# Kernel tuning notes

Measured on AMD Instinct MI355X. Metric: run time of the kernel, lower is better.

Reference implementation:

```python
import jax, jax.numpy as jnp
import numpy as np

EPS = 1e-8  # torch F.cosine_similarity default eps
N, D, K, S = 200000, 512, 32, 1000

def setup_inputs() -> dict:
    key = jax.random.key(0)
    k1, k2, k3 = jax.random.split(key, 3)
    z = jax.random.normal(k1, (N, D), dtype=jnp.float32)
    knn_neighbors = jax.random.randint(k2, (N, K), 0, N)
    sample_indices = jax.random.randint(k3, (S,), 0, N)
    return {"z": z, "knn_neighbors": knn_neighbors, "sample_indices": sample_indices}

def reference(z, knn_neighbors, sample_indices):
    # Gather sampled centers and their neighbor embeddings.
    centers = z[sample_indices]                         # [S, D]
    neigh = z[knn_neighbors[sample_indices]]            # [S, K, D]
    # Cosine similarity along D (torch semantics: dot / max(|a||b|, eps)).
    dot = jnp.einsum('sd,skd->sk', centers, neigh)      # [S, K]
    norm_c = jnp.linalg.norm(centers, axis=-1)          # [S]
    norm_n = jnp.linalg.norm(neigh, axis=-1)            # [S, K]
    cos = dot / jnp.maximum(norm_c[:, None] * norm_n, EPS)
    # Per-center loss 1 - mean cos sim, averaged over sampled centers.
    return jnp.mean(1.0 - jnp.mean(cos, axis=1))
```

## Files before the change

### kernel.cpp

```cpp
#include <hip/hip_runtime.h>
#include <hip/hip_bf16.h>


#define DDIM 512
#define KNN 32
#define EPSV 1e-8f

__global__ __launch_bounds__(256) void ncl_pair_kernel(
    const float* __restrict__ z,
    const int* __restrict__ knn,
    const int* __restrict__ samp,
    float* __restrict__ block_sums) {
    const int b    = blockIdx.x;
    const int s    = b >> 3;
    const int g    = b & 7;
    const int lane = threadIdx.x & 63;
    const int wave = threadIdx.x >> 6;
    const int k    = g * 4 + wave;

    const int cidx = samp[s];
    const int nidx = knn[(size_t)cidx * KNN + k];

    const float4* __restrict__ crow = (const float4*)(z + (size_t)cidx * DDIM);
    const float4* __restrict__ nrow = (const float4*)(z + (size_t)nidx * DDIM);
    const float4 c0 = crow[lane];
    const float4 c1 = crow[64 + lane];
    const float4 n0 = nrow[lane];
    const float4 n1 = nrow[64 + lane];

    float cn = c0.x*c0.x; float dp = c0.x*n0.x; float nn = n0.x*n0.x;
    cn = fmaf(c0.y, c0.y, cn); dp = fmaf(c0.y, n0.y, dp); nn = fmaf(n0.y, n0.y, nn);
    cn = fmaf(c0.z, c0.z, cn); dp = fmaf(c0.z, n0.z, dp); nn = fmaf(n0.z, n0.z, nn);
    cn = fmaf(c0.w, c0.w, cn); dp = fmaf(c0.w, n0.w, dp); nn = fmaf(n0.w, n0.w, nn);
    cn = fmaf(c1.x, c1.x, cn); dp = fmaf(c1.x, n1.x, dp); nn = fmaf(n1.x, n1.x, nn);
    cn = fmaf(c1.y, c1.y, cn); dp = fmaf(c1.y, n1.y, dp); nn = fmaf(n1.y, n1.y, nn);
    cn = fmaf(c1.z, c1.z, cn); dp = fmaf(c1.z, n1.z, dp); nn = fmaf(n1.z, n1.z, nn);
    cn = fmaf(c1.w, c1.w, cn); dp = fmaf(c1.w, n1.w, dp); nn = fmaf(n1.w, n1.w, nn);

    #pragma unroll
    for (int off = 32; off; off >>= 1) {
        cn += __shfl_xor(cn, off, 64);
        dp += __shfl_xor(dp, off, 64);
        nn += __shfl_xor(nn, off, 64);
    }

    __shared__ float red[4];
    if (lane == 0) {
        const float denom = fmaxf(sqrtf(cn) * sqrtf(nn), EPSV);
        red[wave] = dp / denom;
    }
    __syncthreads();
    if (threadIdx.x == 0)
        block_sums[b] = red[0] + red[1] + red[2] + red[3];
}

__global__ __launch_bounds__(256) void ncl_finalize_kernel(
    const float* __restrict__ block_sums, float* __restrict__ out, int nblocks, float inv_sk) {
    __shared__ float red[256];
    float acc = 0.0f;
    for (int i = threadIdx.x; i < nblocks; i += 256) acc += block_sums[i];
    red[threadIdx.x] = acc;
    __syncthreads();
    #pragma unroll
    for (int off = 128; off; off >>= 1) {
        if (threadIdx.x < off) red[threadIdx.x] += red[threadIdx.x + off];
        __syncthreads();
    }
    if (threadIdx.x == 0)
        out[0] = 1.0f - red[0] * inv_sk;
}

extern "C" void kernel_launch(void* const* d_in, const int* in_sizes, int n_in,
                              void* d_out, int out_size, void* d_ws, size_t ws_size,
                              hipStream_t stream) {
    const float* z    = (const float*)d_in[0];
    const int*   knn  = (const int*)d_in[1];
    const int*   samp = (const int*)d_in[2];
    const int    S    = in_sizes[2];
    const int    nblocks = S * 8;

    float* block_sums = (float*)d_ws;
    float* out        = (float*)d_out;

    ncl_pair_kernel<<<nblocks, 256, 0, stream>>>(z, knn, samp, block_sums);
    ncl_finalize_kernel<<<1, 256, 0, stream>>>(block_sums, out, nblocks,
                                               1.0f / ((float)S * (float)KNN));
}
```

Before: 471.0 us.

## Process four neighbors per wave and reuse center row across them

Each wave now gathers four neighbor rows and computes four cosine similarities, sharing a single load of the center row, and the grid shrinks from eight to two blocks per sample. This cuts redundant center-row reads and index loads and puts more independent loads in flight per wave. In exchange there are fewer waves overall and higher register use, which may reduce latency hiding.

```diff
diff --git a/kernel.cpp b/kernel.cpp
--- a/kernel.cpp
+++ b/kernel.cpp
@@ -12,42 +12,70 @@
     const int* __restrict__ samp,
     float* __restrict__ block_sums) {
     const int b    = blockIdx.x;
-    const int s    = b >> 3;
-    const int g    = b & 7;
+    const int s    = b >> 1;
+    const int h    = b & 1;
     const int lane = threadIdx.x & 63;
     const int wave = threadIdx.x >> 6;
-    const int k    = g * 4 + wave;
+    const int kbase = h * 16 + wave * 4;
 
     const int cidx = samp[s];
-    const int nidx = knn[(size_t)cidx * KNN + k];
+    const int* __restrict__ krow = knn + (size_t)cidx * KNN + kbase;
+    const int i0 = krow[0], i1 = krow[1], i2 = krow[2], i3 = krow[3];
 
     const float4* __restrict__ crow = (const float4*)(z + (size_t)cidx * DDIM);
-    const float4* __restrict__ nrow = (const float4*)(z + (size_t)nidx * DDIM);
+    const float4* __restrict__ r0 = (const float4*)(z + (size_t)i0 * DDIM);
+    const float4* __restrict__ r1 = (const float4*)(z + (size_t)i1 * DDIM);
+    const float4* __restrict__ r2 = (const float4*)(z + (size_t)i2 * DDIM);
+    const float4* __restrict__ r3 = (const float4*)(z + (size_t)i3 * DDIM);
+
     const float4 c0 = crow[lane];
     const float4 c1 = crow[64 + lane];
-    const float4 n0 = nrow[lane];
-    const float4 n1 = nrow[64 + lane];
+    const float4 a0 = r0[lane], a1 = r0[64 + lane];
+    const float4 b0 = r1[lane], b1 = r1[64 + lane];
+    const float4 d0 = r2[lane], d1 = r2[64 + lane];
+    const float4 e0 = r3[lane], e1 = r3[64 + lane];
 
-    float cn = c0.x*c0.x; float dp = c0.x*n0.x; float nn = n0.x*n0.x;
-    cn = fmaf(c0.y, c0.y, cn); dp = fmaf(c0.y, n0.y, dp); nn = fmaf(n0.y, n0.y, nn);
-    cn = fmaf(c0.z, c0.z, cn); dp = fmaf(c0.z, n0.z, dp); nn = fmaf(n0.z, n0.z, nn);
-    cn = fmaf(c0.w, c0.w, cn); dp = fmaf(c0.w, n0.w, dp); nn = fmaf(n0.w, n0.w, nn);
-    cn = fmaf(c1.x, c1.x, cn); dp = fmaf(c1.x, n1.x, dp); nn = fmaf(n1.x, n1.x, nn);
-    cn = fmaf(c1.y, c1.y, cn); dp = fmaf(c1.y, n1.y, dp); nn = fmaf(n1.y, n1.y, nn);
-    cn = fmaf(c1.z, c1.z, cn); dp = fmaf(c1.z, n1.z, dp); nn = fmaf(n1.z, n1.z, nn);
-    cn = fmaf(c1.w, c1.w, cn); dp = fmaf(c1.w, n1.w, dp); nn = fmaf(n1.w, n1.w, nn);
+    float cn  = c0.x*c0.x;
+    float dpa = c0.x*a0.x, nna = a0.x*a0.x;
+    float dpb = c0.x*b0.x, nnb = b0.x*b0.x;
+    float dpd = c0.x*d0.x, nnd = d0.x*d0.x;
+    float dpe = c0.x*e0.x, nne = e0.x*e0.x;
+#define ACC(cx, ax, bx, dx, ex)                                        \
+    cn  = fmaf(cx, cx, cn);                                            \
+    dpa = fmaf(cx, ax, dpa); nna = fmaf(ax, ax, nna);                  \
+    dpb = fmaf(cx, bx, dpb); nnb = fmaf(bx, bx, nnb);                  \
+    dpd = fmaf(cx, dx, dpd); nnd = fmaf(dx, dx, nnd);                  \
+    dpe = fmaf(cx, ex, dpe); nne = fmaf(ex, ex, nne);
+    ACC(c0.y, a0.y, b0.y, d0.y, e0.y)
+    ACC(c0.z, a0.z, b0.z, d0.z, e0.z)
+    ACC(c0.w, a0.w, b0.w, d0.w, e0.w)
+    ACC(c1.x, a1.x, b1.x, d1.x, e1.x)
+    ACC(c1.y, a1.y, b1.y, d1.y, e1.y)
+    ACC(c1.z, a1.z, b1.z, d1.z, e1.z)
+    ACC(c1.w, a1.w, b1.w, d1.w, e1.w)
+#undef ACC
 
     #pragma unroll
     for (int off = 32; off; off >>= 1) {
-        cn += __shfl_xor(cn, off, 64);
-        dp += __shfl_xor(dp, off, 64);
-        nn += __shfl_xor(nn, off, 64);
+        cn  += __shfl_xor(cn,  off, 64);
+        dpa += __shfl_xor(dpa, off, 64);
+        nna += __shfl_xor(nna, off, 64);
+        dpb += __shfl_xor(dpb, off, 64);
+        nnb += __shfl_xor(nnb, off, 64);
+        dpd += __shfl_xor(dpd, off, 64);
+        nnd += __shfl_xor(nnd, off, 64);
+        dpe += __shfl_xor(dpe, off, 64);
+        nne += __shfl_xor(nne, off, 64);
     }
 
     __shared__ float red[4];
     if (lane == 0) {
-        const float denom = fmaxf(sqrtf(cn) * sqrtf(nn), EPSV);
-        red[wave] = dp / denom;
+        const float cnorm = sqrtf(cn);
+        float w = dpa / fmaxf(cnorm * sqrtf(nna), EPSV);
+        w      += dpb / fmaxf(cnorm * sqrtf(nnb), EPSV);
+        w      += dpd / fmaxf(cnorm * sqrtf(nnd), EPSV);
+        w      += dpe / fmaxf(cnorm * sqrtf(nne), EPSV);
+        red[wave] = w;
     }
     __syncthreads();
     if (threadIdx.x == 0)
@@ -77,7 +105,7 @@
     const int*   knn  = (const int*)d_in[1];
     const int*   samp = (const int*)d_in[2];
     const int    S    = in_sizes[2];
-    const int    nblocks = S * 8;
+    const int    nblocks = S * 2;
 
     float* block_sums = (float*)d_ws;
     float* out        = (float*)d_out;
```

Measured after the change: 466.7 us. No clear change (-0.9%).
